# Kernel optimization log

Measured on AMD Instinct MI355X. Metric: run time of the kernel, lower is better.

## Reference

```python
import jax, jax.numpy as jnp
import numpy as np

NUM_GRAPHS = 100  # batch of graphs for pooling (dgl.max_nodes / WeightAndSum)


def _glorot(k, shape):
    lim = np.sqrt(6.0 / (shape[0] + shape[1])).astype(np.float32)
    return jax.random.uniform(k, shape, jnp.float32, -lim, lim)


def setup_inputs() -> dict:
    key = jax.random.key(0)
    ks = jax.random.split(key, 10)
    N, E, D, H = 100000, 1600000, 128, 128
    node_feats = jax.random.normal(ks[0], (N, D), dtype=jnp.float32)
    src = jax.random.randint(ks[1], (E,), 0, N, dtype=jnp.int32)
    dst = jax.random.randint(ks[2], (E,), 0, N, dtype=jnp.int32)
    graph_ids = jnp.sort(jax.random.randint(ks[3], (N,), 0, NUM_GRAPHS, dtype=jnp.int32))
    W1 = _glorot(ks[4], (D, H)); b1 = jnp.zeros((H,), jnp.float32)
    W2 = _glorot(ks[5], (H, H)); b2 = jnp.zeros((H,), jnp.float32)
    W3 = _glorot(ks[6], (H, H)); b3 = jnp.zeros((H,), jnp.float32)
    W_pool = _glorot(ks[7], (H, 1)); b_pool = jnp.zeros((1,), jnp.float32)
    return {"node_feats": node_feats, "src": src, "dst": dst, "graph_ids": graph_ids,
            "W1": W1, "b1": b1, "W2": W2, "b2": b2, "W3": W3, "b3": b3,
            "W_pool": W_pool, "b_pool": b_pool}


def _gcn_layer(h, W, b, src, dst, norm_src, norm_dst, N):
    # DGL GraphConv, norm='both': D_dst^{-1/2} (A^T (D_src^{-1/2} X W)) + b
    h = (h * norm_src[:, None]) @ W                      # [N, H]
    agg = jax.ops.segment_sum(h[src], dst, num_segments=N)  # gather + scatter-add
    return agg * norm_dst[:, None] + b


def reference(node_feats, src, dst, graph_ids, W1, b1, W2, b2, W3, b3, W_pool, b_pool):
    N = node_feats.shape[0]
    # dgl.add_self_loop (allow_zero_in_degree=False)
    loops = jnp.arange(N, dtype=src.dtype)
    src_sl = jnp.concatenate([src, loops])
    dst_sl = jnp.concatenate([dst, loops])
    ones = jnp.ones(src_sl.shape, jnp.float32)
    out_deg = jax.ops.segment_sum(ones, src_sl, num_segments=N)
    in_deg = jax.ops.segment_sum(ones, dst_sl, num_segments=N)
    norm_src = jax.lax.rsqrt(jnp.maximum(out_deg, 1.0))
    norm_dst = jax.lax.rsqrt(jnp.maximum(in_deg, 1.0))
    h = node_feats
    for W, b in ((W1, b1), (W2, b2), (W3, b3)):
        h = jax.nn.relu(_gcn_layer(h, W, b, src_sl, dst_sl, norm_src, norm_dst, N))
    # pooling_func: WeightAndSum (sigmoid-gated weighted sum per graph) + max_nodes
    w = jax.nn.sigmoid(h @ W_pool + b_pool)              # [N, 1]
    g_sum = jax.ops.segment_sum(h * w, graph_ids, num_segments=NUM_GRAPHS)
    g_max = jax.ops.segment_max(h, graph_ids, num_segments=NUM_GRAPHS)
    return jnp.concatenate([g_sum, g_max], axis=1)       # [G, 2H]
```

## Files before the change

### kernel.cpp

```cpp
#include <hip/hip_runtime.h>
#include <hip/hip_bf16.h>

#define DIM 128
#define CAP 64
#define NBMAX 64
#define BCAP 36864

typedef __attribute__((ext_vector_type(8))) short bf16x8;
typedef __attribute__((ext_vector_type(4))) float f32x4;
union U16 { uint4 u; bf16x8 b; };

__device__ __forceinline__ unsigned short f2bf(float f) {
    unsigned u = __float_as_uint(f);
    unsigned r = (u + 0x7fffu + ((u >> 16) & 1u)) >> 16;
    return (unsigned short)r;
}
__device__ __forceinline__ unsigned pack2bf(float a, float b) {
    return (unsigned)f2bf(a) | ((unsigned)f2bf(b) << 16);
}
__device__ __forceinline__ float2 unpack2bf(unsigned v) {
    float2 r;
    r.x = __uint_as_float(v << 16);
    r.y = __uint_as_float(v & 0xffff0000u);
    return r;
}
__device__ __forceinline__ void accum8s(float* acc, uint4 v, float s) {
    float2 f0 = unpack2bf(v.x), f1 = unpack2bf(v.y);
    float2 f2 = unpack2bf(v.z), f3 = unpack2bf(v.w);
    acc[0] += s * f0.x; acc[1] += s * f0.y; acc[2] += s * f1.x; acc[3] += s * f1.y;
    acc[4] += s * f2.x; acc[5] += s * f2.y; acc[6] += s * f3.x; acc[7] += s * f3.y;
}

__global__ __launch_bounds__(256) void k_bin(const int* __restrict__ src,
                                             const int* __restrict__ dst, int E,
                                             unsigned* __restrict__ binD,
                                             unsigned short* __restrict__ binS,
                                             int* __restrict__ cntD,
                                             int* __restrict__ cntS, int NB) {
    __shared__ int hD[NBMAX], hS[NBMAX], bD[NBMAX], bS[NBMAX];
    int t = threadIdx.x;
    if (t < NB) { hD[t] = 0; hS[t] = 0; }
    __syncthreads();
    int e0 = blockIdx.x * 1024 + t * 4;
    int s[4], d[4];
    bool v[4];
#pragma unroll
    for (int i = 0; i < 4; i++) {
        v[i] = (e0 + i) < E;
        s[i] = 0; d[i] = 0;
        if (v[i]) { s[i] = src[e0 + i]; d[i] = dst[e0 + i]; }
    }
#pragma unroll
    for (int i = 0; i < 4; i++) {
        if (v[i]) {
            atomicAdd(&hD[d[i] >> 11], 1);
            atomicAdd(&hS[s[i] >> 11], 1);
        }
    }
    __syncthreads();
    if (t < NB) {
        bD[t] = atomicAdd(&cntD[t], hD[t]);
        bS[t] = atomicAdd(&cntS[t], hS[t]);
        hD[t] = 0; hS[t] = 0;
    }
    __syncthreads();
#pragma unroll
    for (int i = 0; i < 4; i++) {
        if (v[i]) {
            int bd = d[i] >> 11;
            int r = atomicAdd(&hD[bd], 1);
            int idx = bD[bd] + r;
            if (idx < BCAP)
                binD[bd * BCAP + idx] = ((unsigned)(d[i] & 2047) << 17) | (unsigned)s[i];
            int bs = s[i] >> 11;
            int r2 = atomicAdd(&hS[bs], 1);
            int idx2 = bS[bs] + r2;
            if (idx2 < BCAP) binS[bs * BCAP + idx2] = (unsigned short)(s[i] & 2047);
        }
    }
}

__global__ __launch_bounds__(256) void k_mega(const unsigned* __restrict__ binD,
                                              const unsigned short* __restrict__ binS,
                                              const int* __restrict__ cntD,
                                              const int* __restrict__ cntS,
                                              int* __restrict__ in_cnt,
                                              int* __restrict__ out_cnt,
                                              int* __restrict__ csr_pad,
                                              const float* __restrict__ x,
                                              const float* __restrict__ W,
                                              unsigned* __restrict__ xwb, int N,
                                              const float* __restrict__ W2,
                                              const float* __restrict__ W3,
                                              unsigned* __restrict__ wT2g,
                                              unsigned* __restrict__ wT3g,
                                              int NB, int nSpec) {
    __shared__ __align__(16) char smem[24576];
    int bid = blockIdx.x;
    int t = threadIdx.x;

    if (bid < NB) {
        int* cnt = (int*)smem;
        for (int j = t; j < 2048; j += 256) cnt[j] = 0;
        __syncthreads();
        int base = bid << 11;
        int nE = cntD[bid];
        if (nE > BCAP) nE = BCAP;
        const unsigned* bb = &binD[bid * BCAP];
        for (int i = t; i < nE; i += 256) {
            unsigned e = bb[i];
            int dl = (int)(e >> 17);
            int sv = (int)(e & 0x1FFFFu);
            int pos = atomicAdd(&cnt[dl], 1);
            if (pos < CAP) csr_pad[(size_t)(base + dl) * CAP + pos] = sv;
        }
        __syncthreads();
        for (int j = t; j < 2048; j += 256) {
            int n = base + j;
            if (n < N) in_cnt[n] = cnt[j];
        }
        return;
    }
    if (bid < 2 * NB) {
        int b = bid - NB;
        int* hist = (int*)smem;
        for (int j = t; j < 2048; j += 256) hist[j] = 0;
        __syncthreads();
        int base = b << 11;
        int nE = cntS[b];
        if (nE > BCAP) nE = BCAP;
        const unsigned short* bs = &binS[b * BCAP];
        for (int i = t; i < nE; i += 256) {
            atomicAdd(&hist[(int)bs[i]], 1);
        }
        __syncthreads();
        for (int j = t; j < 2048; j += 256) {
            int n = base + j;
            if (n < N) out_cnt[n] = hist[j];
        }
        return;
    }
    if (bid < nSpec) {
        const float* Wsrc = (bid - 2 * NB == 0) ? W2 : W3;
        unsigned* wTg = (bid - 2 * NB == 0) ? wT2g : wT3g;
        int n = t >> 1;
        int kp0 = (t & 1) * 32;
#pragma unroll
        for (int i = 0; i < 32; i++) {
            int kp = kp0 + i;
            wTg[n * 64 + kp] = pack2bf(Wsrc[(2 * kp) * DIM + n], Wsrc[(2 * kp + 1) * DIM + n]);
        }
        return;
    }
    int gb = bid - nSpec;
    float (*sW)[128] = (float(*)[128])smem;
    float (*sX)[64] = (float(*)[64])(smem + 16384);
    int ty = t >> 4;
    int tx = t & 15;
    int nodeBase = gb * 64;

    float acc[4][8];
#pragma unroll
    for (int m = 0; m < 4; m++)
#pragma unroll
        for (int j = 0; j < 8; j++) acc[m][j] = 0.f;

    int ln = t & 63;
    int kb = (t >> 6) * 8;
    int nd = nodeBase + ln;

#pragma unroll 1
    for (int kc = 0; kc < DIM; kc += 32) {
#pragma unroll
        for (int i = 0; i < 4; i++) {
            int v = t + i * 256;
            int kk = v >> 5;
            int cc = (v & 31) * 4;
            *(float4*)&sW[kk][cc] = *(const float4*)&W[(kc + kk) * DIM + cc];
        }
        float4 a0, a1;
        if (nd < N) {
            a0 = *(const float4*)&x[nd * DIM + kc + kb];
            a1 = *(const float4*)&x[nd * DIM + kc + kb + 4];
        } else {
            a0 = make_float4(0, 0, 0, 0);
            a1 = make_float4(0, 0, 0, 0);
        }
        sX[kb + 0][ln] = a0.x;
        sX[kb + 1][ln] = a0.y;
        sX[kb + 2][ln] = a0.z;
        sX[kb + 3][ln] = a0.w;
        sX[kb + 4][ln] = a1.x;
        sX[kb + 5][ln] = a1.y;
        sX[kb + 6][ln] = a1.z;
        sX[kb + 7][ln] = a1.w;
        __syncthreads();

#pragma unroll
        for (int k = 0; k < 32; k++) {
            float4 xv = *(float4*)&sX[k][ty * 4];
            float4 wa = *(float4*)&sW[k][tx * 4];
            float4 wb = *(float4*)&sW[k][tx * 4 + 64];
            float xm[4] = {xv.x, xv.y, xv.z, xv.w};
#pragma unroll
            for (int m = 0; m < 4; m++) {
                acc[m][0] += xm[m] * wa.x;
                acc[m][1] += xm[m] * wa.y;
                acc[m][2] += xm[m] * wa.z;
                acc[m][3] += xm[m] * wa.w;
                acc[m][4] += xm[m] * wb.x;
                acc[m][5] += xm[m] * wb.y;
                acc[m][6] += xm[m] * wb.z;
                acc[m][7] += xm[m] * wb.w;
            }
        }
        __syncthreads();
    }

#pragma unroll
    for (int m = 0; m < 4; m++) {
        int n2 = nodeBase + ty * 4 + m;
        if (n2 < N) {
            uint2 q0, q1;
            q0.x = pack2bf(acc[m][0], acc[m][1]);
            q0.y = pack2bf(acc[m][2], acc[m][3]);
            q1.x = pack2bf(acc[m][4], acc[m][5]);
            q1.y = pack2bf(acc[m][6], acc[m][7]);
            *(uint2*)&xwb[n2 * 64 + tx * 2] = q0;
            *(uint2*)&xwb[n2 * 64 + 32 + tx * 2] = q1;
        }
    }
}

__global__ __launch_bounds__(256) void k_agg1(const uint4* __restrict__ xwb4,
                                              const int* __restrict__ in_cnt,
                                              const int* __restrict__ out_cnt,
                                              const int* __restrict__ csr_pad,
                                              const float* __restrict__ bias,
                                              uint4* __restrict__ hb4, int N) {
    int gid = blockIdx.x * blockDim.x + threadIdx.x;
    int n = gid >> 6;
    int lane = gid & 63;
    if (n >= N) return;
    int quad = lane >> 4;
    int c = lane & 15;

    float acc[8];
#pragma unroll
    for (int i = 0; i < 8; i++) acc[i] = 0.f;

    if (quad == 0) {
        float sn = rsqrtf((float)(out_cnt[n] + 1));
        accum8s(acc, xwb4[n * 16 + c], sn);
    }
    int deg_true = in_cnt[n];
    int deg = deg_true > CAP ? CAP : deg_true;
    const int* row = &csr_pad[(size_t)n * CAP];
    int p = 0;
    for (; p + 16 <= deg; p += 16) {
        int s0 = row[p + quad];
        int s1 = row[p + 4 + quad];
        int s2 = row[p + 8 + quad];
        int s3 = row[p + 12 + quad];
        uint4 v0 = xwb4[s0 * 16 + c];
        uint4 v1 = xwb4[s1 * 16 + c];
        uint4 v2 = xwb4[s2 * 16 + c];
        uint4 v3 = xwb4[s3 * 16 + c];
        float n0 = rsqrtf((float)(out_cnt[s0] + 1));
        float n1 = rsqrtf((float)(out_cnt[s1] + 1));
        float n2 = rsqrtf((float)(out_cnt[s2] + 1));
        float n3 = rsqrtf((float)(out_cnt[s3] + 1));
        accum8s(acc, v0, n0);
        accum8s(acc, v1, n1);
        accum8s(acc, v2, n2);
        accum8s(acc, v3, n3);
    }
    for (; p + 8 <= deg; p += 8) {
        int s0 = row[p + quad];
        int s1 = row[p + 4 + quad];
        uint4 v0 = xwb4[s0 * 16 + c];
        uint4 v1 = xwb4[s1 * 16 + c];
        float n0 = rsqrtf((float)(out_cnt[s0] + 1));
        float n1 = rsqrtf((float)(out_cnt[s1] + 1));
        accum8s(acc, v0, n0);
        accum8s(acc, v1, n1);
    }
    for (; p < deg; p += 4) {
        int pe = p + quad;
        int s = row[pe < deg ? pe : p];
        uint4 v = xwb4[s * 16 + c];
        float ns = rsqrtf((float)(out_cnt[s] + 1));
        if (pe < deg) accum8s(acc, v, ns);
    }
#pragma unroll
    for (int i = 0; i < 8; i++) {
        acc[i] += __shfl_xor(acc[i], 16, 64);
        acc[i] += __shfl_xor(acc[i], 32, 64);
    }
    float ndv = rsqrtf((float)(deg_true + 1));
    if (quad == 0) {
        float4 b0 = ((const float4*)bias)[2 * c];
        float4 b1 = ((const float4*)bias)[2 * c + 1];
        uint4 w;
        w.x = pack2bf(fmaxf(acc[0] * ndv + b0.x, 0.f), fmaxf(acc[1] * ndv + b0.y, 0.f));
        w.y = pack2bf(fmaxf(acc[2] * ndv + b0.z, 0.f), fmaxf(acc[3] * ndv + b0.w, 0.f));
        w.z = pack2bf(fmaxf(acc[4] * ndv + b1.x, 0.f), fmaxf(acc[5] * ndv + b1.y, 0.f));
        w.w = pack2bf(fmaxf(acc[6] * ndv + b1.z, 0.f), fmaxf(acc[7] * ndv + b1.w, 0.f));
        hb4[n * 16 + c] = w;
    }
}

__global__ __launch_bounds__(256) void k_xw_mfma(const unsigned* __restrict__ hb,
                                                 const int* __restrict__ out_cnt,
                                                 const unsigned* __restrict__ wTg,
                                                 unsigned* __restrict__ xwb, int N) {
    __shared__ unsigned wT[128 * 68];
    int t = threadIdx.x;
#pragma unroll
    for (int i = 0; i < 8; i++) {
        int idx = t + i * 256;
        int row = idx >> 4;
        int col = idx & 15;
        *(uint4*)&wT[row * 68 + col * 4] = ((const uint4*)wTg)[idx];
    }
    __syncthreads();
    int wave = t >> 6, lane = t & 63;
    int quad = lane >> 4, c = lane & 15;
    int m = blockIdx.x * 64 + wave * 16 + c;
    bool mv = m < N;
    f32x4 acc[8];
#pragma unroll
    for (int i = 0; i < 8; i++) acc[i] = (f32x4){0.f, 0.f, 0.f, 0.f};

#pragma unroll
    for (int ks = 0; ks < 4; ks++) {
        U16 av;
        if (mv) av.u = *(const uint4*)&hb[m * 64 + ks * 16 + quad * 4];
        else av.u = make_uint4(0, 0, 0, 0);
#pragma unroll
        for (int cb = 0; cb < 8; cb++) {
            U16 bv;
            bv.u = *(const uint4*)&wT[(cb * 16 + c) * 68 + ks * 16 + quad * 4];
            acc[cb] = __builtin_amdgcn_mfma_f32_16x16x32_bf16(av.b, bv.b, acc[cb], 0, 0, 0);
        }
    }
    int rowBase = blockIdx.x * 64 + wave * 16 + quad * 4;
#pragma unroll
    for (int r = 0; r < 4; r++) {
        int rowN = rowBase + r;
        float nrm = (rowN < N) ? rsqrtf((float)(out_cnt[rowN] + 1)) : 0.f;
#pragma unroll
        for (int cb = 0; cb < 8; cb++) {
            float v = acc[cb][r] * nrm;
            float vn = __shfl_xor(v, 1, 64);
            if (((c & 1) == 0) && rowN < N)
                xwb[rowN * 64 + cb * 8 + (c >> 1)] = pack2bf(v, vn);
        }
    }
}

template <bool GATED>
__device__ __forceinline__ void agg_body(const uint4* __restrict__ xwb4,
                                         const int* __restrict__ in_cnt,
                                         const int* __restrict__ csr_pad,
                                         const float* __restrict__ bias,
                                         uint4* __restrict__ hb4,
                                         const float* __restrict__ Wp,
                                         const float* __restrict__ bp,
                                         float* __restrict__ wg, int N) {
    int gid = blockIdx.x * blockDim.x + threadIdx.x;
    int n = gid >> 6;
    int lane = gid & 63;
    if (n >= N) return;
    int quad = lane >> 4;
    int c = lane & 15;

    float acc[8];
#pragma unroll
    for (int i = 0; i < 8; i++) acc[i] = 0.f;

    if (quad == 0) {
        accum8s(acc, xwb4[n * 16 + c], 1.f);
    }
    int deg_true = in_cnt[n];
    int deg = deg_true > CAP ? CAP : deg_true;
    const int* row = &csr_pad[(size_t)n * CAP];
    int p = 0;
    for (; p + 16 <= deg; p += 16) {
        int s0 = row[p + quad];
        int s1 = row[p + 4 + quad];
        int s2 = row[p + 8 + quad];
        int s3 = row[p + 12 + quad];
        uint4 v0 = xwb4[s0 * 16 + c];
        uint4 v1 = xwb4[s1 * 16 + c];
        uint4 v2 = xwb4[s2 * 16 + c];
        uint4 v3 = xwb4[s3 * 16 + c];
        accum8s(acc, v0, 1.f);
        accum8s(acc, v1, 1.f);
        accum8s(acc, v2, 1.f);
        accum8s(acc, v3, 1.f);
    }
    for (; p + 8 <= deg; p += 8) {
        int s0 = row[p + quad];
        int s1 = row[p + 4 + quad];
        uint4 v0 = xwb4[s0 * 16 + c];
        uint4 v1 = xwb4[s1 * 16 + c];
        accum8s(acc, v0, 1.f);
        accum8s(acc, v1, 1.f);
    }
    for (; p < deg; p += 4) {
        int pe = p + quad;
        int s = row[pe < deg ? pe : p];
        uint4 v = xwb4[s * 16 + c];
        if (pe < deg) accum8s(acc, v, 1.f);
    }
#pragma unroll
    for (int i = 0; i < 8; i++) {
        acc[i] += __shfl_xor(acc[i], 16, 64);
        acc[i] += __shfl_xor(acc[i], 32, 64);
    }
    float ndv = rsqrtf((float)(deg_true + 1));
    float4 b0 = ((const float4*)bias)[2 * c];
    float4 b1 = ((const float4*)bias)[2 * c + 1];
    float o[8];
    o[0] = fmaxf(acc[0] * ndv + b0.x, 0.f);
    o[1] = fmaxf(acc[1] * ndv + b0.y, 0.f);
    o[2] = fmaxf(acc[2] * ndv + b0.z, 0.f);
    o[3] = fmaxf(acc[3] * ndv + b0.w, 0.f);
    o[4] = fmaxf(acc[4] * ndv + b1.x, 0.f);
    o[5] = fmaxf(acc[5] * ndv + b1.y, 0.f);
    o[6] = fmaxf(acc[6] * ndv + b1.z, 0.f);
    o[7] = fmaxf(acc[7] * ndv + b1.w, 0.f);
    if (quad == 0) {
        uint4 w;
        w.x = pack2bf(o[0], o[1]);
        w.y = pack2bf(o[2], o[3]);
        w.z = pack2bf(o[4], o[5]);
        w.w = pack2bf(o[6], o[7]);
        hb4[n * 16 + c] = w;
    }
    if (GATED) {
        float s = 0.f;
        if (quad == 0) {
            float4 w0 = ((const float4*)Wp)[2 * c];
            float4 w1 = ((const float4*)Wp)[2 * c + 1];
            s = o[0] * w0.x + o[1] * w0.y + o[2] * w0.z + o[3] * w0.w +
                o[4] * w1.x + o[5] * w1.y + o[6] * w1.z + o[7] * w1.w;
        }
        s += __shfl_xor(s, 1, 64);
        s += __shfl_xor(s, 2, 64);
        s += __shfl_xor(s, 4, 64);
        s += __shfl_xor(s, 8, 64);
        if (lane == 0) wg[n] = 1.f / (1.f + expf(-(s + bp[0])));
    }
}

__global__ __launch_bounds__(256) void k_agg(const uint4* __restrict__ xwb4,
                                             const int* __restrict__ in_cnt,
                                             const int* __restrict__ csr_pad,
                                             const float* __restrict__ bias,
                                             uint4* __restrict__ hb4, int N) {
    agg_body<false>(xwb4, in_cnt, csr_pad, bias, hb4, nullptr, nullptr, nullptr, N);
}

__global__ __launch_bounds__(256) void k_agg_gate(const uint4* __restrict__ xwb4,
                                                  const int* __restrict__ in_cnt,
                                                  const int* __restrict__ csr_pad,
                                                  const float* __restrict__ bias,
                                                  uint4* __restrict__ hb4,
                                                  const float* __restrict__ Wp,
                                                  const float* __restrict__ bp,
                                                  float* __restrict__ wg, int N) {
    agg_body<true>(xwb4, in_cnt, csr_pad, bias, hb4, Wp, bp, wg, N);
}

__device__ __forceinline__ int lower_bound(const int* a, int n, int key) {
    int lo = 0, hi = n;
    while (lo < hi) {
        int m = (lo + hi) >> 1;
        if (a[m] < key) lo = m + 1;
        else hi = m;
    }
    return lo;
}

__global__ __launch_bounds__(64) void k_pool(const unsigned* __restrict__ hb,
                                             const float* __restrict__ wg,
                                             const int* __restrict__ gids,
                                             float* __restrict__ out, int N) {
    int g = blockIdx.x >> 4;
    int part = blockIdx.x & 15;
    int t = threadIdx.x;
    int start = lower_bound(gids, N, g);
    int end = lower_bound(gids, N, g + 1);
    float2 sum = {0.f, 0.f}, mx = {0.f, 0.f};
    for (int n = start + part; n < end; n += 16) {
        float w = wg[n];
        float2 v = unpack2bf(hb[n * 64 + t]);
        sum.x += v.x * w;
        sum.y += v.y * w;
        mx.x = fmaxf(mx.x, v.x);
        mx.y = fmaxf(mx.y, v.y);
    }
    atomicAdd(&out[g * 256 + 2 * t], sum.x);
    atomicAdd(&out[g * 256 + 2 * t + 1], sum.y);
    atomicMax((int*)&out[g * 256 + 128 + 2 * t], __float_as_int(mx.x));
    atomicMax((int*)&out[g * 256 + 128 + 2 * t + 1], __float_as_int(mx.y));
}

extern "C" void kernel_launch(void* const* d_in, const int* in_sizes, int n_in,
                              void* d_out, int out_size, void* d_ws, size_t ws_size,
                              hipStream_t stream) {
    const float* node_feats = (const float*)d_in[0];
    const int* src = (const int*)d_in[1];
    const int* dst = (const int*)d_in[2];
    const int* gids = (const int*)d_in[3];
    const float* W1 = (const float*)d_in[4];
    const float* b1 = (const float*)d_in[5];
    const float* W2 = (const float*)d_in[6];
    const float* b2 = (const float*)d_in[7];
    const float* W3 = (const float*)d_in[8];
    const float* b3 = (const float*)d_in[9];
    const float* Wp = (const float*)d_in[10];
    const float* bp = (const float*)d_in[11];
    float* out = (float*)d_out;

    const int N = in_sizes[3];
    const int E = in_sizes[1];
    const int G = out_size / 256;
    const int NB = (N + 2047) >> 11;

    char* ws = (char*)d_ws;
    size_t o = 0;
    int* cntD = (int*)(ws + o);          o += NBMAX * 4;
    int* cntS = (int*)(ws + o);          o += NBMAX * 4;
    size_t zero_bytes = o;
    int* in_cnt = (int*)(ws + o);        o += (size_t)N * 4;
    int* out_cnt = (int*)(ws + o);       o += (size_t)N * 4;
    float* wg = (float*)(ws + o);        o += (size_t)N * 4;
    o = (o + 15) & ~15ull;
    unsigned* wT2g = (unsigned*)(ws + o); o += 8192 * 4;
    unsigned* wT3g = (unsigned*)(ws + o); o += 8192 * 4;
    unsigned* binD = (unsigned*)(ws + o); o += (size_t)NBMAX * BCAP * 4;
    unsigned short* binS = (unsigned short*)(ws + o); o += (size_t)NBMAX * BCAP * 2;
    o = (o + 15) & ~15ull;
    int* csr_pad = (int*)(ws + o);       o += (size_t)N * CAP * 4;
    unsigned* xwb = (unsigned*)(ws + o); o += (size_t)N * 64 * 4;
    unsigned* hb = (unsigned*)(ws + o);  o += (size_t)N * 64 * 4;
    (void)ws_size;

    (void)hipMemsetAsync(d_ws, 0, zero_bytes, stream);
    (void)hipMemsetAsync(d_out, 0, (size_t)out_size * 4, stream);

    int binGrid = (E + 1023) / 1024;
    int mmGrid = (N + 63) / 64;
    int aggGrid = ((N * 64) + 255) / 256;
    int nSpec = 2 * NB + 2;

    k_bin<<<binGrid, 256, 0, stream>>>(src, dst, E, binD, binS, cntD, cntS, NB);
    k_mega<<<nSpec + mmGrid, 256, 0, stream>>>(binD, binS, cntD, cntS, in_cnt, out_cnt,
                                               csr_pad, node_feats, W1, xwb, N,
                                               W2, W3, wT2g, wT3g, NB, nSpec);
    k_agg1<<<aggGrid, 256, 0, stream>>>((const uint4*)xwb, in_cnt, out_cnt, csr_pad, b1,
                                        (uint4*)hb, N);
    k_xw_mfma<<<mmGrid, 256, 0, stream>>>(hb, out_cnt, wT2g, xwb, N);
    k_agg<<<aggGrid, 256, 0, stream>>>((const uint4*)xwb, in_cnt, csr_pad, b2,
                                       (uint4*)hb, N);
    k_xw_mfma<<<mmGrid, 256, 0, stream>>>(hb, out_cnt, wT3g, xwb, N);
    k_agg_gate<<<aggGrid, 256, 0, stream>>>((const uint4*)xwb, in_cnt, csr_pad, b3,
                                            (uint4*)hb, Wp, bp, wg, N);
    k_pool<<<G * 16, 64, 0, stream>>>(hb, wg, gids, out, N);
}
```

Before: 470.4 us.

## Co-schedule edge binning with the first-layer GEMM in one interleaved launch

Merges the edge-binning kernel with the layer-1 dense X·W1 GEMM and the W2/W3 bf16 transposes into a single launch. Odd and even blocks alternate between binning and GEMM work. The CSR build and degree histograms move into their own small kernel. The aim is to overlap the memory-bound, atomic-heavy binning with the compute-bound GEMM so neither leaves the GPU idle. The cost is extra empty blocks when the two grid sizes differ, plus one more kernel launch for the CSR step.

```diff
diff --git a/kernel.cpp b/kernel.cpp
--- a/kernel.cpp
+++ b/kernel.cpp
@@ -31,78 +31,178 @@
     acc[4] += s * f2.x; acc[5] += s * f2.y; acc[6] += s * f3.x; acc[7] += s * f3.y;
 }
 
-__global__ __launch_bounds__(256) void k_bin(const int* __restrict__ src,
-                                             const int* __restrict__ dst, int E,
-                                             unsigned* __restrict__ binD,
-                                             unsigned short* __restrict__ binS,
-                                             int* __restrict__ cntD,
-                                             int* __restrict__ cntS, int NB) {
-    __shared__ int hD[NBMAX], hS[NBMAX], bD[NBMAX], bS[NBMAX];
+__global__ __launch_bounds__(256) void k_bin_gemm(const int* __restrict__ src,
+                                                  const int* __restrict__ dst, int E,
+                                                  unsigned* __restrict__ binD,
+                                                  unsigned short* __restrict__ binS,
+                                                  int* __restrict__ cntD,
+                                                  int* __restrict__ cntS,
+                                                  const float* __restrict__ x,
+                                                  const float* __restrict__ W,
+                                                  unsigned* __restrict__ xwb, int N,
+                                                  const float* __restrict__ W2,
+                                                  const float* __restrict__ W3,
+                                                  unsigned* __restrict__ wT2g,
+                                                  unsigned* __restrict__ wT3g,
+                                                  int binGrid, int mmGrid, int pairGrid,
+                                                  int NB) {
+    __shared__ __align__(16) char smem[24576];
     int t = threadIdx.x;
-    if (t < NB) { hD[t] = 0; hS[t] = 0; }
-    __syncthreads();
-    int e0 = blockIdx.x * 1024 + t * 4;
-    int s[4], d[4];
-    bool v[4];
-#pragma unroll
-    for (int i = 0; i < 4; i++) {
-        v[i] = (e0 + i) < E;
-        s[i] = 0; d[i] = 0;
-        if (v[i]) { s[i] = src[e0 + i]; d[i] = dst[e0 + i]; }
-    }
-#pragma unroll
-    for (int i = 0; i < 4; i++) {
-        if (v[i]) {
-            atomicAdd(&hD[d[i] >> 11], 1);
-            atomicAdd(&hS[s[i] >> 11], 1);
-        }
-    }
-    __syncthreads();
-    if (t < NB) {
-        bD[t] = atomicAdd(&cntD[t], hD[t]);
-        bS[t] = atomicAdd(&cntS[t], hS[t]);
-        hD[t] = 0; hS[t] = 0;
-    }
-    __syncthreads();
-#pragma unroll
-    for (int i = 0; i < 4; i++) {
-        if (v[i]) {
-            int bd = d[i] >> 11;
-            int r = atomicAdd(&hD[bd], 1);
-            int idx = bD[bd] + r;
-            if (idx < BCAP)
-                binD[bd * BCAP + idx] = ((unsigned)(d[i] & 2047) << 17) | (unsigned)s[i];
-            int bs = s[i] >> 11;
-            int r2 = atomicAdd(&hS[bs], 1);
-            int idx2 = bS[bs] + r2;
-            if (idx2 < BCAP) binS[bs * BCAP + idx2] = (unsigned short)(s[i] & 2047);
-        }
-    }
-}
-
-__global__ __launch_bounds__(256) void k_mega(const unsigned* __restrict__ binD,
-                                              const unsigned short* __restrict__ binS,
-                                              const int* __restrict__ cntD,
-                                              const int* __restrict__ cntS,
-                                              int* __restrict__ in_cnt,
-                                              int* __restrict__ out_cnt,
-                                              int* __restrict__ csr_pad,
-                                              const float* __restrict__ x,
-                                              const float* __restrict__ W,
-                                              unsigned* __restrict__ xwb, int N,
-                                              const float* __restrict__ W2,
-                                              const float* __restrict__ W3,
-                                              unsigned* __restrict__ wT2g,
-                                              unsigned* __restrict__ wT3g,
-                                              int NB, int nSpec) {
-    __shared__ __align__(16) char smem[24576];
+    if ((int)blockIdx.x >= 2 * pairGrid) {
+        int w = blockIdx.x - 2 * pairGrid;
+        const float* Wsrc = (w == 0) ? W2 : W3;
+        unsigned* wTg = (w == 0) ? wT2g : wT3g;
+        int n = t >> 1;
+        int kp0 = (t & 1) * 32;
+#pragma unroll
+        for (int i = 0; i < 32; i++) {
+            int kp = kp0 + i;
+            wTg[n * 64 + kp] = pack2bf(Wsrc[(2 * kp) * DIM + n], Wsrc[(2 * kp + 1) * DIM + n]);
+        }
+        return;
+    }
+    if (blockIdx.x & 1) {
+        int bid = blockIdx.x >> 1;
+        if (bid >= binGrid) return;
+        int* hD = (int*)smem;
+        int* hS = (int*)(smem + 256);
+        int* bD = (int*)(smem + 512);
+        int* bS = (int*)(smem + 768);
+        if (t < NB) { hD[t] = 0; hS[t] = 0; }
+        __syncthreads();
+        int e0 = bid * 1024 + t * 4;
+        int s[4], d[4];
+        bool v[4];
+#pragma unroll
+        for (int i = 0; i < 4; i++) {
+            v[i] = (e0 + i) < E;
+            s[i] = 0; d[i] = 0;
+            if (v[i]) { s[i] = src[e0 + i]; d[i] = dst[e0 + i]; }
+        }
+#pragma unroll
+        for (int i = 0; i < 4; i++) {
+            if (v[i]) {
+                atomicAdd(&hD[d[i] >> 11], 1);
+                atomicAdd(&hS[s[i] >> 11], 1);
+            }
+        }
+        __syncthreads();
+        if (t < NB) {
+            bD[t] = atomicAdd(&cntD[t], hD[t]);
+            bS[t] = atomicAdd(&cntS[t], hS[t]);
+            hD[t] = 0; hS[t] = 0;
+        }
+        __syncthreads();
+#pragma unroll
+        for (int i = 0; i < 4; i++) {
+            if (v[i]) {
+                int bd = d[i] >> 11;
+                int r = atomicAdd(&hD[bd], 1);
+                int idx = bD[bd] + r;
+                if (idx < BCAP)
+                    binD[bd * BCAP + idx] = ((unsigned)(d[i] & 2047) << 17) | (unsigned)s[i];
+                int bs = s[i] >> 11;
+                int r2 = atomicAdd(&hS[bs], 1);
+                int idx2 = bS[bs] + r2;
+                if (idx2 < BCAP) binS[bs * BCAP + idx2] = (unsigned short)(s[i] & 2047);
+            }
+        }
+        return;
+    }
+    int bid = blockIdx.x >> 1;
+    if (bid >= mmGrid) return;
+    float (*sW)[128] = (float(*)[128])smem;
+    float (*sX)[64] = (float(*)[64])(smem + 16384);
+    int ty = t >> 4;
+    int tx = t & 15;
+    int nodeBase = bid * 64;
+
+    float acc[4][8];
+#pragma unroll
+    for (int m = 0; m < 4; m++)
+#pragma unroll
+        for (int j = 0; j < 8; j++) acc[m][j] = 0.f;
+
+    int ln = t & 63;
+    int kb = (t >> 6) * 8;
+    int nd = nodeBase + ln;
+
+#pragma unroll 1
+    for (int kc = 0; kc < DIM; kc += 32) {
+#pragma unroll
+        for (int i = 0; i < 4; i++) {
+            int vv = t + i * 256;
+            int kk = vv >> 5;
+            int cc = (vv & 31) * 4;
+            *(float4*)&sW[kk][cc] = *(const float4*)&W[(kc + kk) * DIM + cc];
+        }
+        float4 a0, a1;
+        if (nd < N) {
+            a0 = *(const float4*)&x[nd * DIM + kc + kb];
+            a1 = *(const float4*)&x[nd * DIM + kc + kb + 4];
+        } else {
+            a0 = make_float4(0, 0, 0, 0);
+            a1 = make_float4(0, 0, 0, 0);
+        }
+        sX[kb + 0][ln] = a0.x;
+        sX[kb + 1][ln] = a0.y;
+        sX[kb + 2][ln] = a0.z;
+        sX[kb + 3][ln] = a0.w;
+        sX[kb + 4][ln] = a1.x;
+        sX[kb + 5][ln] = a1.y;
+        sX[kb + 6][ln] = a1.z;
+        sX[kb + 7][ln] = a1.w;
+        __syncthreads();
+
+#pragma unroll
+        for (int k = 0; k < 32; k++) {
+            float4 xv = *(float4*)&sX[k][ty * 4];
+            float4 wa = *(float4*)&sW[k][tx * 4];
+            float4 wb = *(float4*)&sW[k][tx * 4 + 64];
+            float xm[4] = {xv.x, xv.y, xv.z, xv.w};
+#pragma unroll
+            for (int m = 0; m < 4; m++) {
+                acc[m][0] += xm[m] * wa.x;
+                acc[m][1] += xm[m] * wa.y;
+                acc[m][2] += xm[m] * wa.z;
+                acc[m][3] += xm[m] * wa.w;
+                acc[m][4] += xm[m] * wb.x;
+                acc[m][5] += xm[m] * wb.y;
+                acc[m][6] += xm[m] * wb.z;
+                acc[m][7] += xm[m] * wb.w;
+            }
+        }
+        __syncthreads();
+    }
+
+#pragma unroll
+    for (int m = 0; m < 4; m++) {
+        int n2 = nodeBase + ty * 4 + m;
+        if (n2 < N) {
+            uint2 q0, q1;
+            q0.x = pack2bf(acc[m][0], acc[m][1]);
+            q0.y = pack2bf(acc[m][2], acc[m][3]);
+            q1.x = pack2bf(acc[m][4], acc[m][5]);
+            q1.y = pack2bf(acc[m][6], acc[m][7]);
+            *(uint2*)&xwb[n2 * 64 + tx * 2] = q0;
+            *(uint2*)&xwb[n2 * 64 + 32 + tx * 2] = q1;
+        }
+    }
+}
+
+__global__ __launch_bounds__(256) void k_csr(const unsigned* __restrict__ binD,
+                                             const unsigned short* __restrict__ binS,
+                                             const int* __restrict__ cntD,
+                                             const int* __restrict__ cntS,
+                                             int* __restrict__ in_cnt,
+                                             int* __restrict__ out_cnt,
+                                             int* __restrict__ csr_pad, int N, int NB) {
+    __shared__ int cnt[2048];
     int bid = blockIdx.x;
     int t = threadIdx.x;
-
+    for (int j = t; j < 2048; j += 256) cnt[j] = 0;
+    __syncthreads();
     if (bid < NB) {
-        int* cnt = (int*)smem;
-        for (int j = t; j < 2048; j += 256) cnt[j] = 0;
-        __syncthreads();
         int base = bid << 11;
         int nE = cntD[bid];
         if (nE > BCAP) nE = BCAP;
@@ -119,115 +219,19 @@
             int n = base + j;
             if (n < N) in_cnt[n] = cnt[j];
         }
-        return;
-    }
-    if (bid < 2 * NB) {
+    } else {
         int b = bid - NB;
-        int* hist = (int*)smem;
-        for (int j = t; j < 2048; j += 256) hist[j] = 0;
-        __syncthreads();
         int base = b << 11;
         int nE = cntS[b];
         if (nE > BCAP) nE = BCAP;
         const unsigned short* bs = &binS[b * BCAP];
         for (int i = t; i < nE; i += 256) {
-            atomicAdd(&hist[(int)bs[i]], 1);
+            atomicAdd(&cnt[(int)bs[i]], 1);
         }
         __syncthreads();
         for (int j = t; j < 2048; j += 256) {
             int n = base + j;
-            if (n < N) out_cnt[n] = hist[j];
-        }
-        return;
-    }
-    if (bid < nSpec) {
-        const float* Wsrc = (bid - 2 * NB == 0) ? W2 : W3;
-        unsigned* wTg = (bid - 2 * NB == 0) ? wT2g : wT3g;
-        int n = t >> 1;
-        int kp0 = (t & 1) * 32;
-#pragma unroll
-        for (int i = 0; i < 32; i++) {
-            int kp = kp0 + i;
-            wTg[n * 64 + kp] = pack2bf(Wsrc[(2 * kp) * DIM + n], Wsrc[(2 * kp + 1) * DIM + n]);
-        }
-        return;
-    }
-    int gb = bid - nSpec;
-    float (*sW)[128] = (float(*)[128])smem;
-    float (*sX)[64] = (float(*)[64])(smem + 16384);
-    int ty = t >> 4;
-    int tx = t & 15;
-    int nodeBase = gb * 64;
-
-    float acc[4][8];
-#pragma unroll
-    for (int m = 0; m < 4; m++)
-#pragma unroll
-        for (int j = 0; j < 8; j++) acc[m][j] = 0.f;
-
-    int ln = t & 63;
-    int kb = (t >> 6) * 8;
-    int nd = nodeBase + ln;
-
-#pragma unroll 1
-    for (int kc = 0; kc < DIM; kc += 32) {
-#pragma unroll
-        for (int i = 0; i < 4; i++) {
-            int v = t + i * 256;
-            int kk = v >> 5;
-            int cc = (v & 31) * 4;
-            *(float4*)&sW[kk][cc] = *(const float4*)&W[(kc + kk) * DIM + cc];
-        }
-        float4 a0, a1;
-        if (nd < N) {
-            a0 = *(const float4*)&x[nd * DIM + kc + kb];
-            a1 = *(const float4*)&x[nd * DIM + kc + kb + 4];
-        } else {
-            a0 = make_float4(0, 0, 0, 0);
-            a1 = make_float4(0, 0, 0, 0);
-        }
-        sX[kb + 0][ln] = a0.x;
-        sX[kb + 1][ln] = a0.y;
-        sX[kb + 2][ln] = a0.z;
-        sX[kb + 3][ln] = a0.w;
-        sX[kb + 4][ln] = a1.x;
-        sX[kb + 5][ln] = a1.y;
-        sX[kb + 6][ln] = a1.z;
-        sX[kb + 7][ln] = a1.w;
-        __syncthreads();
-
-#pragma unroll
-        for (int k = 0; k < 32; k++) {
-            float4 xv = *(float4*)&sX[k][ty * 4];
-            float4 wa = *(float4*)&sW[k][tx * 4];
-            float4 wb = *(float4*)&sW[k][tx * 4 + 64];
-            float xm[4] = {xv.x, xv.y, xv.z, xv.w};
-#pragma unroll
-            for (int m = 0; m < 4; m++) {
-                acc[m][0] += xm[m] * wa.x;
-                acc[m][1] += xm[m] * wa.y;
-                acc[m][2] += xm[m] * wa.z;
-                acc[m][3] += xm[m] * wa.w;
-                acc[m][4] += xm[m] * wb.x;
-                acc[m][5] += xm[m] * wb.y;
-                acc[m][6] += xm[m] * wb.z;
-                acc[m][7] += xm[m] * wb.w;
-            }
-        }
-        __syncthreads();
-    }
-
-#pragma unroll
-    for (int m = 0; m < 4; m++) {
-        int n2 = nodeBase + ty * 4 + m;
-        if (n2 < N) {
-            uint2 q0, q1;
-            q0.x = pack2bf(acc[m][0], acc[m][1]);
-            q0.y = pack2bf(acc[m][2], acc[m][3]);
-            q1.x = pack2bf(acc[m][4], acc[m][5]);
-            q1.y = pack2bf(acc[m][6], acc[m][7]);
-            *(uint2*)&xwb[n2 * 64 + tx * 2] = q0;
-            *(uint2*)&xwb[n2 * 64 + 32 + tx * 2] = q1;
+            if (n < N) out_cnt[n] = cnt[j];
         }
     }
 }
@@ -555,12 +559,14 @@
     int binGrid = (E + 1023) / 1024;
     int mmGrid = (N + 63) / 64;
     int aggGrid = ((N * 64) + 255) / 256;
-    int nSpec = 2 * NB + 2;
-
-    k_bin<<<binGrid, 256, 0, stream>>>(src, dst, E, binD, binS, cntD, cntS, NB);
-    k_mega<<<nSpec + mmGrid, 256, 0, stream>>>(binD, binS, cntD, cntS, in_cnt, out_cnt,
-                                               csr_pad, node_feats, W1, xwb, N,
-                                               W2, W3, wT2g, wT3g, NB, nSpec);
+    int pairGrid = binGrid > mmGrid ? binGrid : mmGrid;
+
+    k_bin_gemm<<<2 * pairGrid + 2, 256, 0, stream>>>(src, dst, E, binD, binS, cntD, cntS,
+                                                     node_feats, W1, xwb, N,
+                                                     W2, W3, wT2g, wT3g,
+                                                     binGrid, mmGrid, pairGrid, NB);
+    k_csr<<<2 * NB, 256, 0, stream>>>(binD, binS, cntD, cntS, in_cnt, out_cnt,
+                                      csr_pad, N, NB);
     k_agg1<<<aggGrid, 256, 0, stream>>>((const uint4*)xwb, in_cnt, out_cnt, csr_pad, b1,
                                         (uint4*)hb, N);
     k_xw_mfma<<<mmGrid, 256, 0, stream>>>(hb, out_cnt, wT2g, xwb, N);
```

After: 500.3 us. 6.3% more time.
